# Kernel tuning notes

Hardware: AMD Instinct MI355X
Metric: run time of the kernel (lower is better)

## Reference

```python
import jax, jax.numpy as jnp
import numpy as np

IN_DIM = 2
HID = 256
OUT_DIM = 1
B = 131072


def setup_inputs() -> dict:
    key = jax.random.key(0)
    ks = jax.random.split(key, 9)
    def glorot(k, shape):
        fan_in = shape[0]
        return jax.random.normal(k, shape, dtype=jnp.float32) / jnp.sqrt(jnp.float32(fan_in))
    return {
        "x": jax.random.normal(ks[0], (B, IN_DIM), dtype=jnp.float32),
        "W1": glorot(ks[1], (IN_DIM, HID)), "b1": jnp.zeros((HID,), jnp.float32),
        "W2": glorot(ks[2], (HID, HID)),    "b2": jnp.zeros((HID,), jnp.float32),
        "W3": glorot(ks[3], (HID, HID)),    "b3": jnp.zeros((HID,), jnp.float32),
        "W4": glorot(ks[4], (HID, OUT_DIM)),"b4": jnp.zeros((OUT_DIM,), jnp.float32),
    }


def reference(x, W1, b1, W2, b2, W3, b3, W4, b4):
    # Inner PINN model: tanh MLP, per-sample fn (IN_DIM,) -> (OUT_DIM,)
    def f(xi):
        h = jnp.tanh(xi @ W1 + b1)
        h = jnp.tanh(h @ W2 + b2)
        h = jnp.tanh(h @ W3 + b3)
        return h @ W4 + b4

    # Original layer computes full batch_jacobian then slices column 0.
    # Mathematically this is the directional derivative along e0, computed
    # here directly with forward-mode JVPs (same values, no wasted columns).
    e0 = jnp.zeros((IN_DIM,), x.dtype).at[0].set(1.0)

    def du_dx0(xi):  # (OUT_DIM,) : d u / d x[0]
        return jax.jvp(f, (xi,), (e0,))[1]

    def per_point(xi):
        u = f(xi)                                   # (OUT_DIM,)
        du, d2u = jax.jvp(du_dx0, (xi,), (e0,))     # du/dx0, d2u/dx0^2
        return u, du, d2u

    return jax.vmap(per_point)(x)  # each (B, OUT_DIM)
```

## Files before the change

### kernel.cpp

```cpp
#include <hip/hip_runtime.h>


#define HID 256
#define TM  32
#define LDK 264

typedef _Float16 half8 __attribute__((ext_vector_type(8)));
typedef _Float16 half4 __attribute__((ext_vector_type(4)));
typedef float    f32x4  __attribute__((ext_vector_type(4)));
typedef float    f32x16 __attribute__((ext_vector_type(16)));

__device__ __forceinline__ float fast_tanh(float z) {
    const float e = __expf(2.0f * z);
#if __has_builtin(__builtin_amdgcn_rcpf)
    const float r = __builtin_amdgcn_rcpf(e + 1.0f);
#else
    const float r = 1.0f / (e + 1.0f);
#endif
    return fmaf(-2.0f, r, 1.0f);
}

__device__ __forceinline__ void wait_flag(int* f) {
    while (__hip_atomic_load(f, __ATOMIC_ACQUIRE, __HIP_MEMORY_SCOPE_WORKGROUP) == 0)
        __builtin_amdgcn_s_sleep(1);
}
__device__ __forceinline__ void set_flag(int* f) {
    __hip_atomic_store(f, 1, __ATOMIC_RELEASE, __HIP_MEMORY_SCOPE_WORKGROUP);
}

__global__ __launch_bounds__(256) void prep_w(const float* __restrict__ W2,
                                              const float* __restrict__ W3,
                                              _Float16* __restrict__ wsf) {
    const int t = blockIdx.x * 256 + threadIdx.x;
    const float* __restrict__ W = (t >> 13) ? W3 : W2;
    _Float16* dst = wsf + (size_t)(t >> 13) * 65536;
    const int r    = t & 8191;
    const int s    = r >> 10;
    const int c    = (r >> 6) & 15;
    const int lane = r & 63;
    const int row0 = c * 16 + ((lane >> 5) << 3);
    const int col  = s * 32 + (lane & 31);
    half8 vh;
    #pragma unroll
    for (int j = 0; j < 8; ++j)
        vh[j] = (_Float16)W[(size_t)(row0 + j) * HID + col];
    *(half8*)&dst[(size_t)r * 8] = vh;
}

__global__ __launch_bounds__(512) void pinn_mfma(
    const float* __restrict__ x,
    const float* __restrict__ W1, const float* __restrict__ b1,
    const float* __restrict__ b2, const float* __restrict__ b3,
    const float* __restrict__ W4, const float* __restrict__ b4,
    const _Float16* __restrict__ wsf,
    float* __restrict__ out, int B)
{
    __shared__ __align__(16) _Float16 buf1[3][TM][LDK];
    __shared__ __align__(16) _Float16 buf2[3][TM][LDK];
    __shared__ float psum[8][3][TM];
    __shared__ int flag1[8];
    __shared__ int flag2[8];

    const int tid  = threadIdx.x;
    const int s0   = blockIdx.x * TM;
    const int lane = tid & 63;
    const int wave = tid >> 6;
    const int n    = lane & 31;
    const int q    = lane >> 5;
    const int q8   = q * 8;

    if (tid < 8) { flag1[tid] = 0; flag2[tid] = 0; }
    __syncthreads();

    {
        const int u0 = wave * 32 + q * 16;
        const float x0 = x[(s0 + n) * 2 + 0];
        const float x1 = x[(s0 + n) * 2 + 1];
        #pragma unroll
        for (int g = 0; g < 4; ++g) {
            const f32x4 wa = *(const f32x4*)&W1[u0 + g * 4];
            const f32x4 wb = *(const f32x4*)&W1[HID + u0 + g * 4];
            const f32x4 bv = *(const f32x4*)&b1[u0 + g * 4];
            half4 h0, h1, h2;
            #pragma unroll
            for (int r = 0; r < 4; ++r) {
                const float z  = fmaf(x0, wa[r], fmaf(x1, wb[r], bv[r]));
                const float a  = fast_tanh(z);
                const float sN = 1.0f - a * a;
                const float ad  = sN * wa[r];
                const float add = -2.0f * a * ad * wa[r];
                h0[r] = (_Float16)a;
                h1[r] = (_Float16)ad;
                h2[r] = (_Float16)add;
            }
            *(half4*)&buf1[0][n][u0 + g * 4] = h0;
            *(half4*)&buf1[1][n][u0 + g * 4] = h1;
            *(half4*)&buf1[2][n][u0 + g * 4] = h2;
        }
    }
    if (lane == 0) set_flag(&flag1[wave]);

    f32x16 acc0, acc1, acc2;

    {
        const _Float16* __restrict__ Wp = wsf;
        #pragma unroll
        for (int e = 0; e < 16; ++e) { acc0[e] = 0.f; acc1[e] = 0.f; acc2[e] = 0.f; }

        #define WIDX(c) (((size_t)(wave * 16 + (c)) * 64 + lane) * 8)
        half8 wA = *(const half8*)&Wp[WIDX(2 * wave)];
        half8 wB = *(const half8*)&Wp[WIDX(2 * wave + 1)];
        #pragma unroll
        for (int i = 0; i < 8; ++i) {
            const int p = (wave + i) & 7;
            half8 wAn, wBn;
            if (i < 7) {
                const int pn = (wave + i + 1) & 7;
                wAn = *(const half8*)&Wp[WIDX(2 * pn)];
                wBn = *(const half8*)&Wp[WIDX(2 * pn + 1)];
            }
            if (i) wait_flag(&flag1[p]);
            {
                const int cc = 2 * p;
                const half8 b0 = *(const half8*)&buf1[0][n][cc * 16 + q8];
                const half8 b1f = *(const half8*)&buf1[1][n][cc * 16 + q8];
                const half8 b2f = *(const half8*)&buf1[2][n][cc * 16 + q8];
                acc0 = __builtin_amdgcn_mfma_f32_32x32x16_f16(wA, b0,  acc0, 0, 0, 0);
                acc1 = __builtin_amdgcn_mfma_f32_32x32x16_f16(wA, b1f, acc1, 0, 0, 0);
                acc2 = __builtin_amdgcn_mfma_f32_32x32x16_f16(wA, b2f, acc2, 0, 0, 0);
            }
            {
                const int cc = 2 * p + 1;
                const half8 b0 = *(const half8*)&buf1[0][n][cc * 16 + q8];
                const half8 b1f = *(const half8*)&buf1[1][n][cc * 16 + q8];
                const half8 b2f = *(const half8*)&buf1[2][n][cc * 16 + q8];
                acc0 = __builtin_amdgcn_mfma_f32_32x32x16_f16(wB, b0,  acc0, 0, 0, 0);
                acc1 = __builtin_amdgcn_mfma_f32_32x32x16_f16(wB, b1f, acc1, 0, 0, 0);
                acc2 = __builtin_amdgcn_mfma_f32_32x32x16_f16(wB, b2f, acc2, 0, 0, 0);
            }
            wA = wAn; wB = wBn;
        }
    }

    #pragma unroll
    for (int g = 0; g < 4; ++g) {
        const int ub = wave * 32 + g * 8 + q * 4;
        const f32x4 bb = *(const f32x4*)&b2[ub];
        half4 h0, h1, h2;
        #pragma unroll
        for (int r = 0; r < 4; ++r) {
            const float z   = acc0[g * 4 + r] + bb[r];
            const float a   = fast_tanh(z);
            const float sN  = 1.0f - a * a;
            const float zd  = acc1[g * 4 + r];
            const float zdd = acc2[g * 4 + r];
            const float ad  = sN * zd;
            const float add = fmaf(sN, zdd, -2.0f * a * ad * zd);
            h0[r] = (_Float16)a;
            h1[r] = (_Float16)ad;
            h2[r] = (_Float16)add;
        }
        *(half4*)&buf2[0][n][ub] = h0;
        *(half4*)&buf2[1][n][ub] = h1;
        *(half4*)&buf2[2][n][ub] = h2;
    }
    if (lane == 0) set_flag(&flag2[wave]);

    {
        const _Float16* __restrict__ Wp = wsf + 65536;
        #pragma unroll
        for (int e = 0; e < 16; ++e) { acc0[e] = 0.f; acc1[e] = 0.f; acc2[e] = 0.f; }

        half8 wA = *(const half8*)&Wp[WIDX(2 * wave)];
        half8 wB = *(const half8*)&Wp[WIDX(2 * wave + 1)];
        #pragma unroll
        for (int i = 0; i < 8; ++i) {
            const int p = (wave + i) & 7;
            half8 wAn, wBn;
            if (i < 7) {
                const int pn = (wave + i + 1) & 7;
                wAn = *(const half8*)&Wp[WIDX(2 * pn)];
                wBn = *(const half8*)&Wp[WIDX(2 * pn + 1)];
            }
            if (i) wait_flag(&flag2[p]);
            {
                const int cc = 2 * p;
                const half8 b0 = *(const half8*)&buf2[0][n][cc * 16 + q8];
                const half8 b1f = *(const half8*)&buf2[1][n][cc * 16 + q8];
                const half8 b2f = *(const half8*)&buf2[2][n][cc * 16 + q8];
                acc0 = __builtin_amdgcn_mfma_f32_32x32x16_f16(wA, b0,  acc0, 0, 0, 0);
                acc1 = __builtin_amdgcn_mfma_f32_32x32x16_f16(wA, b1f, acc1, 0, 0, 0);
                acc2 = __builtin_amdgcn_mfma_f32_32x32x16_f16(wA, b2f, acc2, 0, 0, 0);
            }
            {
                const int cc = 2 * p + 1;
                const half8 b0 = *(const half8*)&buf2[0][n][cc * 16 + q8];
                const half8 b1f = *(const half8*)&buf2[1][n][cc * 16 + q8];
                const half8 b2f = *(const half8*)&buf2[2][n][cc * 16 + q8];
                acc0 = __builtin_amdgcn_mfma_f32_32x32x16_f16(wB, b0,  acc0, 0, 0, 0);
                acc1 = __builtin_amdgcn_mfma_f32_32x32x16_f16(wB, b1f, acc1, 0, 0, 0);
                acc2 = __builtin_amdgcn_mfma_f32_32x32x16_f16(wB, b2f, acc2, 0, 0, 0);
            }
            wA = wAn; wB = wBn;
        }
        #undef WIDX
    }

    {
        float pd0 = 0.f, pd1 = 0.f, pd2 = 0.f;
        #pragma unroll
        for (int g = 0; g < 4; ++g) {
            const int ub = wave * 32 + g * 8 + q * 4;
            const f32x4 bb = *(const f32x4*)&b3[ub];
            const f32x4 w4 = *(const f32x4*)&W4[ub];
            #pragma unroll
            for (int r = 0; r < 4; ++r) {
                const float z   = acc0[g * 4 + r] + bb[r];
                const float a   = fast_tanh(z);
                const float sN  = 1.0f - a * a;
                const float zd  = acc1[g * 4 + r];
                const float zdd = acc2[g * 4 + r];
                const float ad  = sN * zd;
                const float add = fmaf(sN, zdd, -2.0f * a * ad * zd);
                pd0 = fmaf(a,   w4[r], pd0);
                pd1 = fmaf(ad,  w4[r], pd1);
                pd2 = fmaf(add, w4[r], pd2);
            }
        }
        pd0 += __shfl_xor(pd0, 32, 64);
        pd1 += __shfl_xor(pd1, 32, 64);
        pd2 += __shfl_xor(pd2, 32, 64);
        if (lane < 32) {
            psum[wave][0][lane] = pd0;
            psum[wave][1][lane] = pd1;
            psum[wave][2][lane] = pd2;
        }
    }
    __syncthreads();

    if (tid < 96) {
        const int s = tid >> 5;
        const int m = tid & 31;
        float v = 0.f;
        #pragma unroll
        for (int w = 0; w < 8; ++w) v += psum[w][s][m];
        if (s == 0) v += b4[0];
        out[(size_t)s * B + s0 + m] = v;
    }
}

extern "C" void kernel_launch(void* const* d_in, const int* in_sizes, int n_in,
                              void* d_out, int out_size, void* d_ws, size_t ws_size,
                              hipStream_t stream) {
    const float* x  = (const float*)d_in[0];
    const float* W1 = (const float*)d_in[1];
    const float* b1 = (const float*)d_in[2];
    const float* W2 = (const float*)d_in[3];
    const float* b2 = (const float*)d_in[4];
    const float* W3 = (const float*)d_in[5];
    const float* b3 = (const float*)d_in[6];
    const float* W4 = (const float*)d_in[7];
    const float* b4 = (const float*)d_in[8];
    float* out = (float*)d_out;

    const int B = in_sizes[0] / 2;

    prep_w<<<64, 256, 0, stream>>>(W2, W3, (_Float16*)d_ws);
    pinn_mfma<<<B / TM, 512, 0, stream>>>(x, W1, b1, b2, b3, W4, b4,
                                          (const _Float16*)d_ws, out, B);
}
```

Baseline: 200.0 us.

## Replace per-wave LDS flags with block barriers and share one LDS buffer

Removes the per-wave flag spin-wait handoff between layers and uses __syncthreads barriers instead. A single LDS activation buffer is now reused for both hidden layers and for the partial-sum reduction, roughly halving shared memory per block so more blocks can be resident. The K loop becomes a simple sequential 16-chunk loop with a one-step weight prefetch. In exchange, the fine-grained overlap of early waves starting the next GEMM before all waves finish is lost, and two extra barriers are added.

Result: faster. 196.0 us (-2.0%).

```diff
diff --git a/kernel.cpp b/kernel.cpp
--- a/kernel.cpp
+++ b/kernel.cpp
@@ -18,14 +18,6 @@
     const float r = 1.0f / (e + 1.0f);
 #endif
     return fmaf(-2.0f, r, 1.0f);
-}
-
-__device__ __forceinline__ void wait_flag(int* f) {
-    while (__hip_atomic_load(f, __ATOMIC_ACQUIRE, __HIP_MEMORY_SCOPE_WORKGROUP) == 0)
-        __builtin_amdgcn_s_sleep(1);
-}
-__device__ __forceinline__ void set_flag(int* f) {
-    __hip_atomic_store(f, 1, __ATOMIC_RELEASE, __HIP_MEMORY_SCOPE_WORKGROUP);
 }
 
 __global__ __launch_bounds__(256) void prep_w(const float* __restrict__ W2,
@@ -55,11 +47,8 @@
     const _Float16* __restrict__ wsf,
     float* __restrict__ out, int B)
 {
-    __shared__ __align__(16) _Float16 buf1[3][TM][LDK];
-    __shared__ __align__(16) _Float16 buf2[3][TM][LDK];
-    __shared__ float psum[8][3][TM];
-    __shared__ int flag1[8];
-    __shared__ int flag2[8];
+    __shared__ __align__(16) _Float16 buf[3][TM][LDK];
+    float* const psum = (float*)&buf[0][0][0];
 
     const int tid  = threadIdx.x;
     const int s0   = blockIdx.x * TM;
@@ -69,13 +58,9 @@
     const int q    = lane >> 5;
     const int q8   = q * 8;
 
-    if (tid < 8) { flag1[tid] = 0; flag2[tid] = 0; }
-    __syncthreads();
-
     {
         const int u0 = wave * 32 + q * 16;
-        const float x0 = x[(s0 + n) * 2 + 0];
-        const float x1 = x[(s0 + n) * 2 + 1];
+        const float2 xv = *(const float2*)&x[(size_t)(s0 + n) * 2];
         #pragma unroll
         for (int g = 0; g < 4; ++g) {
             const f32x4 wa = *(const f32x4*)&W1[u0 + g * 4];
@@ -84,7 +69,7 @@
             half4 h0, h1, h2;
             #pragma unroll
             for (int r = 0; r < 4; ++r) {
-                const float z  = fmaf(x0, wa[r], fmaf(x1, wb[r], bv[r]));
+                const float z  = fmaf(xv.x, wa[r], fmaf(xv.y, wb[r], bv[r]));
                 const float a  = fast_tanh(z);
                 const float sN = 1.0f - a * a;
                 const float ad  = sN * wa[r];
@@ -93,54 +78,36 @@
                 h1[r] = (_Float16)ad;
                 h2[r] = (_Float16)add;
             }
-            *(half4*)&buf1[0][n][u0 + g * 4] = h0;
-            *(half4*)&buf1[1][n][u0 + g * 4] = h1;
-            *(half4*)&buf1[2][n][u0 + g * 4] = h2;
-        }
-    }
-    if (lane == 0) set_flag(&flag1[wave]);
+            *(half4*)&buf[0][n][u0 + g * 4] = h0;
+            *(half4*)&buf[1][n][u0 + g * 4] = h1;
+            *(half4*)&buf[2][n][u0 + g * 4] = h2;
+        }
+    }
+    __syncthreads();
 
     f32x16 acc0, acc1, acc2;
+    #define WIDX(c) (((size_t)(wave * 16 + (c)) * 64 + lane) * 8)
 
     {
         const _Float16* __restrict__ Wp = wsf;
         #pragma unroll
         for (int e = 0; e < 16; ++e) { acc0[e] = 0.f; acc1[e] = 0.f; acc2[e] = 0.f; }
 
-        #define WIDX(c) (((size_t)(wave * 16 + (c)) * 64 + lane) * 8)
-        half8 wA = *(const half8*)&Wp[WIDX(2 * wave)];
-        half8 wB = *(const half8*)&Wp[WIDX(2 * wave + 1)];
-        #pragma unroll
-        for (int i = 0; i < 8; ++i) {
-            const int p = (wave + i) & 7;
-            half8 wAn, wBn;
-            if (i < 7) {
-                const int pn = (wave + i + 1) & 7;
-                wAn = *(const half8*)&Wp[WIDX(2 * pn)];
-                wBn = *(const half8*)&Wp[WIDX(2 * pn + 1)];
-            }
-            if (i) wait_flag(&flag1[p]);
-            {
-                const int cc = 2 * p;
-                const half8 b0 = *(const half8*)&buf1[0][n][cc * 16 + q8];
-                const half8 b1f = *(const half8*)&buf1[1][n][cc * 16 + q8];
-                const half8 b2f = *(const half8*)&buf1[2][n][cc * 16 + q8];
-                acc0 = __builtin_amdgcn_mfma_f32_32x32x16_f16(wA, b0,  acc0, 0, 0, 0);
-                acc1 = __builtin_amdgcn_mfma_f32_32x32x16_f16(wA, b1f, acc1, 0, 0, 0);
-                acc2 = __builtin_amdgcn_mfma_f32_32x32x16_f16(wA, b2f, acc2, 0, 0, 0);
-            }
-            {
-                const int cc = 2 * p + 1;
-                const half8 b0 = *(const half8*)&buf1[0][n][cc * 16 + q8];
-                const half8 b1f = *(const half8*)&buf1[1][n][cc * 16 + q8];
-                const half8 b2f = *(const half8*)&buf1[2][n][cc * 16 + q8];
-                acc0 = __builtin_amdgcn_mfma_f32_32x32x16_f16(wB, b0,  acc0, 0, 0, 0);
-                acc1 = __builtin_amdgcn_mfma_f32_32x32x16_f16(wB, b1f, acc1, 0, 0, 0);
-                acc2 = __builtin_amdgcn_mfma_f32_32x32x16_f16(wB, b2f, acc2, 0, 0, 0);
-            }
-            wA = wAn; wB = wBn;
-        }
-    }
+        half8 wcur = *(const half8*)&Wp[WIDX(0)];
+        #pragma unroll 4
+        for (int c = 0; c < 16; ++c) {
+            half8 wnext;
+            if (c < 15) wnext = *(const half8*)&Wp[WIDX(c + 1)];
+            const half8 b0 = *(const half8*)&buf[0][n][c * 16 + q8];
+            const half8 b1f = *(const half8*)&buf[1][n][c * 16 + q8];
+            const half8 b2f = *(const half8*)&buf[2][n][c * 16 + q8];
+            acc0 = __builtin_amdgcn_mfma_f32_32x32x16_f16(wcur, b0,  acc0, 0, 0, 0);
+            acc1 = __builtin_amdgcn_mfma_f32_32x32x16_f16(wcur, b1f, acc1, 0, 0, 0);
+            acc2 = __builtin_amdgcn_mfma_f32_32x32x16_f16(wcur, b2f, acc2, 0, 0, 0);
+            wcur = wnext;
+        }
+    }
+    __syncthreads();
 
     #pragma unroll
     for (int g = 0; g < 4; ++g) {
@@ -160,81 +127,62 @@
             h1[r] = (_Float16)ad;
             h2[r] = (_Float16)add;
         }
-        *(half4*)&buf2[0][n][ub] = h0;
-        *(half4*)&buf2[1][n][ub] = h1;
-        *(half4*)&buf2[2][n][ub] = h2;
-    }
-    if (lane == 0) set_flag(&flag2[wave]);
+        *(half4*)&buf[0][n][ub] = h0;
+        *(half4*)&buf[1][n][ub] = h1;
+        *(half4*)&buf[2][n][ub] = h2;
+    }
+    __syncthreads();
 
     {
         const _Float16* __restrict__ Wp = wsf + 65536;
         #pragma unroll
         for (int e = 0; e < 16; ++e) { acc0[e] = 0.f; acc1[e] = 0.f; acc2[e] = 0.f; }
 
-        half8 wA = *(const half8*)&Wp[WIDX(2 * wave)];
-        half8 wB = *(const half8*)&Wp[WIDX(2 * wave + 1)];
-        #pragma unroll
-        for (int i = 0; i < 8; ++i) {
-            const int p = (wave + i) & 7;
-            half8 wAn, wBn;
-            if (i < 7) {
-                const int pn = (wave + i + 1) & 7;
-                wAn = *(const half8*)&Wp[WIDX(2 * pn)];
-                wBn = *(const half8*)&Wp[WIDX(2 * pn + 1)];
-            }
-            if (i) wait_flag(&flag2[p]);
-            {
-                const int cc = 2 * p;
-                const half8 b0 = *(const half8*)&buf2[0][n][cc * 16 + q8];
-                const half8 b1f = *(const half8*)&buf2[1][n][cc * 16 + q8];
-                const half8 b2f = *(const half8*)&buf2[2][n][cc * 16 + q8];
-                acc0 = __builtin_amdgcn_mfma_f32_32x32x16_f16(wA, b0,  acc0, 0, 0, 0);
-                acc1 = __builtin_amdgcn_mfma_f32_32x32x16_f16(wA, b1f, acc1, 0, 0, 0);
-                acc2 = __builtin_amdgcn_mfma_f32_32x32x16_f16(wA, b2f, acc2, 0, 0, 0);
-            }
-            {
-                const int cc = 2 * p + 1;
-                const half8 b0 = *(const half8*)&buf2[0][n][cc * 16 + q8];
-                const half8 b1f = *(const half8*)&buf2[1][n][cc * 16 + q8];
-                const half8 b2f = *(const half8*)&buf2[2][n][cc * 16 + q8];
-                acc0 = __builtin_amdgcn_mfma_f32_32x32x16_f16(wB, b0,  acc0, 0, 0, 0);
-                acc1 = __builtin_amdgcn_mfma_f32_32x32x16_f16(wB, b1f, acc1, 0, 0, 0);
-                acc2 = __builtin_amdgcn_mfma_f32_32x32x16_f16(wB, b2f, acc2, 0, 0, 0);
-            }
-            wA = wAn; wB = wBn;
-        }
-        #undef WIDX
-    }
-
-    {
-        float pd0 = 0.f, pd1 = 0.f, pd2 = 0.f;
-        #pragma unroll
-        for (int g = 0; g < 4; ++g) {
-            const int ub = wave * 32 + g * 8 + q * 4;
-            const f32x4 bb = *(const f32x4*)&b3[ub];
-            const f32x4 w4 = *(const f32x4*)&W4[ub];
-            #pragma unroll
-            for (int r = 0; r < 4; ++r) {
-                const float z   = acc0[g * 4 + r] + bb[r];
-                const float a   = fast_tanh(z);
-                const float sN  = 1.0f - a * a;
-                const float zd  = acc1[g * 4 + r];
-                const float zdd = acc2[g * 4 + r];
-                const float ad  = sN * zd;
-                const float add = fmaf(sN, zdd, -2.0f * a * ad * zd);
-                pd0 = fmaf(a,   w4[r], pd0);
-                pd1 = fmaf(ad,  w4[r], pd1);
-                pd2 = fmaf(add, w4[r], pd2);
-            }
-        }
-        pd0 += __shfl_xor(pd0, 32, 64);
-        pd1 += __shfl_xor(pd1, 32, 64);
-        pd2 += __shfl_xor(pd2, 32, 64);
-        if (lane < 32) {
-            psum[wave][0][lane] = pd0;
-            psum[wave][1][lane] = pd1;
-            psum[wave][2][lane] = pd2;
-        }
+        half8 wcur = *(const half8*)&Wp[WIDX(0)];
+        #pragma unroll 4
+        for (int c = 0; c < 16; ++c) {
+            half8 wnext;
+            if (c < 15) wnext = *(const half8*)&Wp[WIDX(c + 1)];
+            const half8 b0 = *(const half8*)&buf[0][n][c * 16 + q8];
+            const half8 b1f = *(const half8*)&buf[1][n][c * 16 + q8];
+            const half8 b2f = *(const half8*)&buf[2][n][c * 16 + q8];
+            acc0 = __builtin_amdgcn_mfma_f32_32x32x16_f16(wcur, b0,  acc0, 0, 0, 0);
+            acc1 = __builtin_amdgcn_mfma_f32_32x32x16_f16(wcur, b1f, acc1, 0, 0, 0);
+            acc2 = __builtin_amdgcn_mfma_f32_32x32x16_f16(wcur, b2f, acc2, 0, 0, 0);
+            wcur = wnext;
+        }
+    }
+    #undef WIDX
+
+    float pd0 = 0.f, pd1 = 0.f, pd2 = 0.f;
+    #pragma unroll
+    for (int g = 0; g < 4; ++g) {
+        const int ub = wave * 32 + g * 8 + q * 4;
+        const f32x4 bb = *(const f32x4*)&b3[ub];
+        const f32x4 w4 = *(const f32x4*)&W4[ub];
+        #pragma unroll
+        for (int r = 0; r < 4; ++r) {
+            const float z   = acc0[g * 4 + r] + bb[r];
+            const float a   = fast_tanh(z);
+            const float sN  = 1.0f - a * a;
+            const float zd  = acc1[g * 4 + r];
+            const float zdd = acc2[g * 4 + r];
+            const float ad  = sN * zd;
+            const float add = fmaf(sN, zdd, -2.0f * a * ad * zd);
+            pd0 = fmaf(a,   w4[r], pd0);
+            pd1 = fmaf(ad,  w4[r], pd1);
+            pd2 = fmaf(add, w4[r], pd2);
+        }
+    }
+    pd0 += __shfl_xor(pd0, 32, 64);
+    pd1 += __shfl_xor(pd1, 32, 64);
+    pd2 += __shfl_xor(pd2, 32, 64);
+
+    __syncthreads();
+    if (lane < 32) {
+        psum[wave * 96 +      lane] = pd0;
+        psum[wave * 96 + 32 + lane] = pd1;
+        psum[wave * 96 + 64 + lane] = pd2;
     }
     __syncthreads();
 
@@ -243,7 +191,7 @@
         const int m = tid & 31;
         float v = 0.f;
         #pragma unroll
-        for (int w = 0; w < 8; ++w) v += psum[w][s][m];
+        for (int w = 0; w < 8; ++w) v += psum[w * 96 + s * 32 + m];
         if (s == 0) v += b4[0];
         out[(size_t)s * B + s0 + m] = v;
     }
```

## Share one LDS activation buffer across layers using reader-count flags

Applied to the files above, without the earlier changes.

Merges the two per-layer LDS activation buffers into a single buffer, roughly halving shared-memory use per block so more blocks can be resident per CU. Per-wave read counters record when all eight waves have consumed a slice of the layer-1 activations. Each wave now computes its layer-2 activations into registers, waits for its counter to reach eight, then overwrites its slice. The loop order also rotates so every wave, including for its own slice, waits on a flag. The costs are extra atomics and spin waits plus more live registers for the held activations.

Measured after the change: 191.9 us. 4.1% less time.

```diff
diff --git a/kernel.cpp b/kernel.cpp
--- a/kernel.cpp
+++ b/kernel.cpp
@@ -20,12 +20,19 @@
     return fmaf(-2.0f, r, 1.0f);
 }
 
-__device__ __forceinline__ void wait_flag(int* f) {
+__device__ __forceinline__ void flag_set(int* f) {
+    __hip_atomic_store(f, 1, __ATOMIC_RELEASE, __HIP_MEMORY_SCOPE_WORKGROUP);
+}
+__device__ __forceinline__ void flag_wait(int* f) {
     while (__hip_atomic_load(f, __ATOMIC_ACQUIRE, __HIP_MEMORY_SCOPE_WORKGROUP) == 0)
         __builtin_amdgcn_s_sleep(1);
 }
-__device__ __forceinline__ void set_flag(int* f) {
-    __hip_atomic_store(f, 1, __ATOMIC_RELEASE, __HIP_MEMORY_SCOPE_WORKGROUP);
+__device__ __forceinline__ void cnt_inc(int* c) {
+    __hip_atomic_fetch_add(c, 1, __ATOMIC_RELEASE, __HIP_MEMORY_SCOPE_WORKGROUP);
+}
+__device__ __forceinline__ void cnt_wait8(int* c) {
+    while (__hip_atomic_load(c, __ATOMIC_ACQUIRE, __HIP_MEMORY_SCOPE_WORKGROUP) < 8)
+        __builtin_amdgcn_s_sleep(1);
 }
 
 __global__ __launch_bounds__(256) void prep_w(const float* __restrict__ W2,
@@ -55,11 +62,9 @@
     const _Float16* __restrict__ wsf,
     float* __restrict__ out, int B)
 {
-    __shared__ __align__(16) _Float16 buf1[3][TM][LDK];
-    __shared__ __align__(16) _Float16 buf2[3][TM][LDK];
+    __shared__ __align__(16) _Float16 buf[3][TM][LDK];
     __shared__ float psum[8][3][TM];
-    __shared__ int flag1[8];
-    __shared__ int flag2[8];
+    __shared__ int pr1[8], rd1[8], pr2[8];
 
     const int tid  = threadIdx.x;
     const int s0   = blockIdx.x * TM;
@@ -69,13 +74,12 @@
     const int q    = lane >> 5;
     const int q8   = q * 8;
 
-    if (tid < 8) { flag1[tid] = 0; flag2[tid] = 0; }
+    if (tid < 8) { pr1[tid] = 0; rd1[tid] = 0; pr2[tid] = 0; }
     __syncthreads();
 
     {
         const int u0 = wave * 32 + q * 16;
-        const float x0 = x[(s0 + n) * 2 + 0];
-        const float x1 = x[(s0 + n) * 2 + 1];
+        const float2 xv = *(const float2*)&x[(size_t)(s0 + n) * 2];
         #pragma unroll
         for (int g = 0; g < 4; ++g) {
             const f32x4 wa = *(const f32x4*)&W1[u0 + g * 4];
@@ -84,7 +88,7 @@
             half4 h0, h1, h2;
             #pragma unroll
             for (int r = 0; r < 4; ++r) {
-                const float z  = fmaf(x0, wa[r], fmaf(x1, wb[r], bv[r]));
+                const float z  = fmaf(xv.x, wa[r], fmaf(xv.y, wb[r], bv[r]));
                 const float a  = fast_tanh(z);
                 const float sN = 1.0f - a * a;
                 const float ad  = sN * wa[r];
@@ -93,126 +97,63 @@
                 h1[r] = (_Float16)ad;
                 h2[r] = (_Float16)add;
             }
-            *(half4*)&buf1[0][n][u0 + g * 4] = h0;
-            *(half4*)&buf1[1][n][u0 + g * 4] = h1;
-            *(half4*)&buf1[2][n][u0 + g * 4] = h2;
-        }
-    }
-    if (lane == 0) set_flag(&flag1[wave]);
+            *(half4*)&buf[0][n][u0 + g * 4] = h0;
+            *(half4*)&buf[1][n][u0 + g * 4] = h1;
+            *(half4*)&buf[2][n][u0 + g * 4] = h2;
+        }
+    }
+    if (lane == 0) flag_set(&pr1[wave]);
 
     f32x16 acc0, acc1, acc2;
+    #define WIDX(c) (((size_t)(wave * 16 + (c)) * 64 + lane) * 8)
 
     {
         const _Float16* __restrict__ Wp = wsf;
         #pragma unroll
         for (int e = 0; e < 16; ++e) { acc0[e] = 0.f; acc1[e] = 0.f; acc2[e] = 0.f; }
 
-        #define WIDX(c) (((size_t)(wave * 16 + (c)) * 64 + lane) * 8)
-        half8 wA = *(const half8*)&Wp[WIDX(2 * wave)];
-        half8 wB = *(const half8*)&Wp[WIDX(2 * wave + 1)];
+        const int p0 = (wave + 1) & 7;
+        half8 wA = *(const half8*)&Wp[WIDX(2 * p0)];
+        half8 wB = *(const half8*)&Wp[WIDX(2 * p0 + 1)];
         #pragma unroll
         for (int i = 0; i < 8; ++i) {
-            const int p = (wave + i) & 7;
+            const int p = (wave + 1 + i) & 7;
             half8 wAn, wBn;
             if (i < 7) {
-                const int pn = (wave + i + 1) & 7;
+                const int pn = (wave + 2 + i) & 7;
                 wAn = *(const half8*)&Wp[WIDX(2 * pn)];
                 wBn = *(const half8*)&Wp[WIDX(2 * pn + 1)];
             }
-            if (i) wait_flag(&flag1[p]);
+            flag_wait(&pr1[p]);
             {
                 const int cc = 2 * p;
-                const half8 b0 = *(const half8*)&buf1[0][n][cc * 16 + q8];
-                const half8 b1f = *(const half8*)&buf1[1][n][cc * 16 + q8];
-                const half8 b2f = *(const half8*)&buf1[2][n][cc * 16 + q8];
+                const half8 b0  = *(const half8*)&buf[0][n][cc * 16 + q8];
+                const half8 b1f = *(const half8*)&buf[1][n][cc * 16 + q8];
+                const half8 b2f = *(const half8*)&buf[2][n][cc * 16 + q8];
                 acc0 = __builtin_amdgcn_mfma_f32_32x32x16_f16(wA, b0,  acc0, 0, 0, 0);
                 acc1 = __builtin_amdgcn_mfma_f32_32x32x16_f16(wA, b1f, acc1, 0, 0, 0);
                 acc2 = __builtin_amdgcn_mfma_f32_32x32x16_f16(wA, b2f, acc2, 0, 0, 0);
             }
             {
                 const int cc = 2 * p + 1;
-                const half8 b0 = *(const half8*)&buf1[0][n][cc * 16 + q8];
-                const half8 b1f = *(const half8*)&buf1[1][n][cc * 16 + q8];
-                const half8 b2f = *(const half8*)&buf1[2][n][cc * 16 + q8];
+                const half8 b0  = *(const half8*)&buf[0][n][cc * 16 + q8];
+                const half8 b1f = *(const half8*)&buf[1][n][cc * 16 + q8];
+                const half8 b2f = *(const half8*)&buf[2][n][cc * 16 + q8];
                 acc0 = __builtin_amdgcn_mfma_f32_32x32x16_f16(wB, b0,  acc0, 0, 0, 0);
                 acc1 = __builtin_amdgcn_mfma_f32_32x32x16_f16(wB, b1f, acc1, 0, 0, 0);
                 acc2 = __builtin_amdgcn_mfma_f32_32x32x16_f16(wB, b2f, acc2, 0, 0, 0);
             }
+            if (lane == 0) cnt_inc(&rd1[p]);
             wA = wAn; wB = wBn;
         }
     }
 
-    #pragma unroll
-    for (int g = 0; g < 4; ++g) {
-        const int ub = wave * 32 + g * 8 + q * 4;
-        const f32x4 bb = *(const f32x4*)&b2[ub];
-        half4 h0, h1, h2;
-        #pragma unroll
-        for (int r = 0; r < 4; ++r) {
-            const float z   = acc0[g * 4 + r] + bb[r];
-            const float a   = fast_tanh(z);
-            const float sN  = 1.0f - a * a;
-            const float zd  = acc1[g * 4 + r];
-            const float zdd = acc2[g * 4 + r];
-            const float ad  = sN * zd;
-            const float add = fmaf(sN, zdd, -2.0f * a * ad * zd);
-            h0[r] = (_Float16)a;
-            h1[r] = (_Float16)ad;
-            h2[r] = (_Float16)add;
-        }
-        *(half4*)&buf2[0][n][ub] = h0;
-        *(half4*)&buf2[1][n][ub] = h1;
-        *(half4*)&buf2[2][n][ub] = h2;
-    }
-    if (lane == 0) set_flag(&flag2[wave]);
-
-    {
-        const _Float16* __restrict__ Wp = wsf + 65536;
-        #pragma unroll
-        for (int e = 0; e < 16; ++e) { acc0[e] = 0.f; acc1[e] = 0.f; acc2[e] = 0.f; }
-
-        half8 wA = *(const half8*)&Wp[WIDX(2 * wave)];
-        half8 wB = *(const half8*)&Wp[WIDX(2 * wave + 1)];
-        #pragma unroll
-        for (int i = 0; i < 8; ++i) {
-            const int p = (wave + i) & 7;
-            half8 wAn, wBn;
-            if (i < 7) {
-                const int pn = (wave + i + 1) & 7;
-                wAn = *(const half8*)&Wp[WIDX(2 * pn)];
-                wBn = *(const half8*)&Wp[WIDX(2 * pn + 1)];
-            }
-            if (i) wait_flag(&flag2[p]);
-            {
-                const int cc = 2 * p;
-                const half8 b0 = *(const half8*)&buf2[0][n][cc * 16 + q8];
-                const half8 b1f = *(const half8*)&buf2[1][n][cc * 16 + q8];
-                const half8 b2f = *(const half8*)&buf2[2][n][cc * 16 + q8];
-                acc0 = __builtin_amdgcn_mfma_f32_32x32x16_f16(wA, b0,  acc0, 0, 0, 0);
-                acc1 = __builtin_amdgcn_mfma_f32_32x32x16_f16(wA, b1f, acc1, 0, 0, 0);
-                acc2 = __builtin_amdgcn_mfma_f32_32x32x16_f16(wA, b2f, acc2, 0, 0, 0);
-            }
-            {
-                const int cc = 2 * p + 1;
-                const half8 b0 = *(const half8*)&buf2[0][n][cc * 16 + q8];
-                const half8 b1f = *(const half8*)&buf2[1][n][cc * 16 + q8];
-                const half8 b2f = *(const half8*)&buf2[2][n][cc * 16 + q8];
-                acc0 = __builtin_amdgcn_mfma_f32_32x32x16_f16(wB, b0,  acc0, 0, 0, 0);
-                acc1 = __builtin_amdgcn_mfma_f32_32x32x16_f16(wB, b1f, acc1, 0, 0, 0);
-                acc2 = __builtin_amdgcn_mfma_f32_32x32x16_f16(wB, b2f, acc2, 0, 0, 0);
-            }
-            wA = wAn; wB = wBn;
-        }
-        #undef WIDX
-    }
-
-    {
-        float pd0 = 0.f, pd1 = 0.f, pd2 = 0.f;
+    {
+        float na[16], nd[16], n2[16];
         #pragma unroll
         for (int g = 0; g < 4; ++g) {
             const int ub = wave * 32 + g * 8 + q * 4;
-            const f32x4 bb = *(const f32x4*)&b3[ub];
-            const f32x4 w4 = *(const f32x4*)&W4[ub];
+            const f32x4 bb = *(const f32x4*)&b2[ub];
             #pragma unroll
             for (int r = 0; r < 4; ++r) {
                 const float z   = acc0[g * 4 + r] + bb[r];
@@ -222,19 +163,95 @@
                 const float zdd = acc2[g * 4 + r];
                 const float ad  = sN * zd;
                 const float add = fmaf(sN, zdd, -2.0f * a * ad * zd);
-                pd0 = fmaf(a,   w4[r], pd0);
-                pd1 = fmaf(ad,  w4[r], pd1);
-                pd2 = fmaf(add, w4[r], pd2);
-            }
-        }
-        pd0 += __shfl_xor(pd0, 32, 64);
-        pd1 += __shfl_xor(pd1, 32, 64);
-        pd2 += __shfl_xor(pd2, 32, 64);
-        if (lane < 32) {
-            psum[wave][0][lane] = pd0;
-            psum[wave][1][lane] = pd1;
-            psum[wave][2][lane] = pd2;
-        }
+                na[g * 4 + r] = a; nd[g * 4 + r] = ad; n2[g * 4 + r] = add;
+            }
+        }
+        cnt_wait8(&rd1[wave]);
+        #pragma unroll
+        for (int g = 0; g < 4; ++g) {
+            const int ub = wave * 32 + g * 8 + q * 4;
+            half4 h0, h1, h2;
+            #pragma unroll
+            for (int r = 0; r < 4; ++r) {
+                h0[r] = (_Float16)na[g * 4 + r];
+                h1[r] = (_Float16)nd[g * 4 + r];
+                h2[r] = (_Float16)n2[g * 4 + r];
+            }
+            *(half4*)&buf[0][n][ub] = h0;
+            *(half4*)&buf[1][n][ub] = h1;
+            *(half4*)&buf[2][n][ub] = h2;
+        }
+    }
+    if (lane == 0) flag_set(&pr2[wave]);
+
+    {
+        const _Float16* __restrict__ Wp = wsf + 65536;
+        #pragma unroll
+        for (int e = 0; e < 16; ++e) { acc0[e] = 0.f; acc1[e] = 0.f; acc2[e] = 0.f; }
+
+        const int p0 = (wave + 1) & 7;
+        half8 wA = *(const half8*)&Wp[WIDX(2 * p0)];
+        half8 wB = *(const half8*)&Wp[WIDX(2 * p0 + 1)];
+        #pragma unroll
+        for (int i = 0; i < 8; ++i) {
+            const int p = (wave + 1 + i) & 7;
+            half8 wAn, wBn;
+            if (i < 7) {
+                const int pn = (wave + 2 + i) & 7;
+                wAn = *(const half8*)&Wp[WIDX(2 * pn)];
+                wBn = *(const half8*)&Wp[WIDX(2 * pn + 1)];
+            }
+            flag_wait(&pr2[p]);
+            {
+                const int cc = 2 * p;
+                const half8 b0  = *(const half8*)&buf[0][n][cc * 16 + q8];
+                const half8 b1f = *(const half8*)&buf[1][n][cc * 16 + q8];
+                const half8 b2f = *(const half8*)&buf[2][n][cc * 16 + q8];
+                acc0 = __builtin_amdgcn_mfma_f32_32x32x16_f16(wA, b0,  acc0, 0, 0, 0);
+                acc1 = __builtin_amdgcn_mfma_f32_32x32x16_f16(wA, b1f, acc1, 0, 0, 0);
+                acc2 = __builtin_amdgcn_mfma_f32_32x32x16_f16(wA, b2f, acc2, 0, 0, 0);
+            }
+            {
+                const int cc = 2 * p + 1;
+                const half8 b0  = *(const half8*)&buf[0][n][cc * 16 + q8];
+                const half8 b1f = *(const half8*)&buf[1][n][cc * 16 + q8];
+                const half8 b2f = *(const half8*)&buf[2][n][cc * 16 + q8];
+                acc0 = __builtin_amdgcn_mfma_f32_32x32x16_f16(wB, b0,  acc0, 0, 0, 0);
+                acc1 = __builtin_amdgcn_mfma_f32_32x32x16_f16(wB, b1f, acc1, 0, 0, 0);
+                acc2 = __builtin_amdgcn_mfma_f32_32x32x16_f16(wB, b2f, acc2, 0, 0, 0);
+            }
+            wA = wAn; wB = wBn;
+        }
+    }
+    #undef WIDX
+
+    float pd0 = 0.f, pd1 = 0.f, pd2 = 0.f;
+    #pragma unroll
+    for (int g = 0; g < 4; ++g) {
+        const int ub = wave * 32 + g * 8 + q * 4;
+        const f32x4 bb = *(const f32x4*)&b3[ub];
+        const f32x4 w4 = *(const f32x4*)&W4[ub];
+        #pragma unroll
+        for (int r = 0; r < 4; ++r) {
+            const float z   = acc0[g * 4 + r] + bb[r];
+            const float a   = fast_tanh(z);
+            const float sN  = 1.0f - a * a;
+            const float zd  = acc1[g * 4 + r];
+            const float zdd = acc2[g * 4 + r];
+            const float ad  = sN * zd;
+            const float add = fmaf(sN, zdd, -2.0f * a * ad * zd);
+            pd0 = fmaf(a,   w4[r], pd0);
+            pd1 = fmaf(ad,  w4[r], pd1);
+            pd2 = fmaf(add, w4[r], pd2);
+        }
+    }
+    pd0 += __shfl_xor(pd0, 32, 64);
+    pd1 += __shfl_xor(pd1, 32, 64);
+    pd2 += __shfl_xor(pd2, 32, 64);
+    if (lane < 32) {
+        psum[wave][0][lane] = pd0;
+        psum[wave][1][lane] = pd1;
+        psum[wave][2][lane] = pd2;
     }
     __syncthreads();
 
```
